# Optimization experiments

Hardware: AMD Instinct MI355X
Metric: run time of the kernel (lower is better)

Reference implementation:

```python
import jax, jax.numpy as jnp
import numpy as np

B, C, H, W = 8, 64, 48, 48
W_SCALE = 0.05  # ~1/sqrt(fan_in=128)


def conv1x1(x, w, b):
    # x: [B, Cin, H, W], w: [Cout, Cin], b: [Cout]
    return jnp.einsum('oc,bchw->bohw', w, x) + b[None, :, None, None]


def setup_inputs() -> dict:
    key = jax.random.key(0)
    ks = jax.random.split(key, 12)
    n = lambda k, s, sc=1.0: jax.random.normal(k, s, dtype=jnp.float32) * sc
    return {
        'xlh': n(ks[0], (B, C, H, W)),
        'xll': n(ks[1], (B, C, H, W)),
        'xrh': n(ks[2], (B, C, H, W)),
        'xrl': n(ks[3], (B, C, H, W)),
        'concaL_w': n(ks[4], (C, 2 * C), W_SCALE), 'concaL_b': jnp.zeros((C,), jnp.float32),
        'concaR_w': n(ks[5], (C, 2 * C), W_SCALE), 'concaR_b': jnp.zeros((C,), jnp.float32),
        'gateL_w': n(ks[6], (1, C), W_SCALE), 'gateL_b': jnp.zeros((1,), jnp.float32),
        'gateR_w': n(ks[7], (1, C), W_SCALE), 'gateR_b': jnp.zeros((1,), jnp.float32),
        'concaLo_w': n(ks[8], (C, 2 * C), W_SCALE), 'concaLo_b': jnp.zeros((C,), jnp.float32),
        'concaRo_w': n(ks[9], (C, 2 * C), W_SCALE), 'concaRo_b': jnp.zeros((C,), jnp.float32),
    }


def reference(xlh, xll, xrh, xrl,
              concaL_w, concaL_b, concaR_w, concaR_b,
              gateL_w, gateL_b, gateR_w, gateR_b,
              concaLo_w, concaLo_b, concaRo_w, concaRo_b):
    xL = conv1x1(jnp.concatenate([xlh, xll], axis=1), concaL_w, concaL_b)  # [B,C,H,W]
    xR = conv1x1(jnp.concatenate([xrh, xrl], axis=1), concaR_w, concaR_b)
    bs, ch, hei, wei = xL.shape
    hw = hei * wei
    xLr = xL.reshape(bs, ch, hw)  # [B,C,HW]
    xRr = xR.reshape(bs, ch, hw)
    # Affinity = xL^T xR : [B, HW_L, HW_R]
    aff = jnp.einsum('bcn,bcm->bnm', xLr, xRr)
    a1 = jax.nn.softmax(aff, axis=1)  # softmax over left positions
    a2 = jax.nn.softmax(aff, axis=2)  # softmax over right positions
    # Branch1: xL @ a1 -> [B,C,HW]
    b1 = jnp.einsum('bcn,bnm->bcm', xLr, a1).reshape(bs, ch, hei, wei)
    g1 = jax.nn.sigmoid(conv1x1(b1, gateL_w, gateL_b))  # [B,1,H,W]
    b1 = b1 * g1
    # Branch2: xR @ a2 -> [B,C,HW]
    b2 = jnp.einsum('bcn,bnm->bcm', xRr, a2).reshape(bs, ch, hei, wei)
    g2 = jax.nn.sigmoid(conv1x1(b2, gateR_w, gateR_b))
    b2 = b2 * g2
    out_L = conv1x1(jnp.concatenate([xL, b1], axis=1), concaLo_w, concaLo_b)
    out_R = conv1x1(jnp.concatenate([xR, b2], axis=1), concaRo_w, concaRo_b)
    return (out_L, out_R)
```

## Files before the change

### kernel.cpp

```cpp
#include <hip/hip_runtime.h>

typedef unsigned short u16;
typedef __bf16 bf16_t;
typedef bf16_t bf16x8 __attribute__((ext_vector_type(8)));
typedef float f32x4 __attribute__((ext_vector_type(4)));

#define B_   8
#define CH   64
#define HW   2304
#define L2E  1.4426950408889634f

#define OFF_XLC   0u
#define OFF_XRC   2359296u
#define OFF_XLT   4718592u
#define OFF_XRT   7077888u
#define OFF_B1    9437184u
#define OFF_B2    14155776u
#define OFF_RS2   18874368u

__device__ __forceinline__ float bf2f(u16 u){
  union { unsigned int i; float f; } v; v.i = ((unsigned int)u) << 16; return v.f;
}
__device__ __forceinline__ u16 f2bf(float f){
  union { float f; unsigned int i; } v; v.f = f;
  unsigned int r = v.i + 0x7FFFu + ((v.i >> 16) & 1u);
  return (u16)(r >> 16);
}
__device__ __forceinline__ void gload16(const void* g, void* l){
  __builtin_amdgcn_global_load_lds(
      (const __attribute__((address_space(1))) void*)g,
      (__attribute__((address_space(3))) void*)l, 16, 0, 0);
}

__global__ __launch_bounds__(256) void k_proj(
    const float* xlh, const float* xll, const float* xrh, const float* xrl,
    const float* wLl, const float* bLl, const float* wRr, const float* bRr,
    char* ws)
{
  int bid = blockIdx.x;
  int b   = bid & 7;
  int q   = bid >> 3;
  int o0  = (q & 3) * 16;
  int side= (q >> 2) & 1;
  int p   = (q >> 3) * 256 + threadIdx.x;
  const float* xh = (side ? xrh : xlh) + (size_t)b*CH*HW;
  const float* xl = (side ? xrl : xll) + (size_t)b*CH*HW;
  const float* w  = (side ? wRr : wLl);
  const float* bi = (side ? bRr : bLl);

  float acc[16];
  #pragma unroll
  for (int j=0;j<16;j++) acc[j] = bi[o0+j];
  for (int c=0;c<64;c++){
    float xv = xh[(size_t)c*HW + p];
    #pragma unroll
    for (int j=0;j<16;j++) acc[j] = fmaf(w[(size_t)(o0+j)*128 + c], xv, acc[j]);
  }
  for (int c=0;c<64;c++){
    float xv = xl[(size_t)c*HW + p];
    #pragma unroll
    for (int j=0;j<16;j++) acc[j] = fmaf(w[(size_t)(o0+j)*128 + 64 + c], xv, acc[j]);
  }
  u16* xc = (u16*)(ws + (side ? OFF_XRC : OFF_XLC)) + (size_t)b*CH*HW;
  u16* xt = (u16*)(ws + (side ? OFF_XRT : OFF_XLT)) + (size_t)b*HW*CH;
  unsigned int pk[8];
  #pragma unroll
  for (int j=0;j<8;j++){
    unsigned int lo16 = f2bf(acc[2*j]);
    unsigned int hi16 = f2bf(acc[2*j+1]);
    pk[j] = lo16 | (hi16 << 16);
    xc[(size_t)(o0+2*j  )*HW + p] = (u16)lo16;
    xc[(size_t)(o0+2*j+1)*HW + p] = (u16)hi16;
  }
  uint4* dst = (uint4*)&xt[(size_t)p*CH + o0];
  dst[0] = make_uint4(pk[0],pk[1],pk[2],pk[3]);
  dst[1] = make_uint4(pk[4],pk[5],pk[6],pk[7]);
}

__global__ __launch_bounds__(256, 4) void k_stats(char* ws)
{
  __shared__ alignas(16) char smraw[16384];
  __shared__ float part[4][4][4];
  int bid = blockIdx.x;
  int b   = bid & 7;
  int r0  = (bid >> 3) * 16;
  const char* Xb = ws + OFF_XLT + (size_t)b*HW*CH*2;
  const char* Yb = ws + OFF_XRT + (size_t)b*HW*CH*2;
  float* out = (float*)(ws + OFF_RS2) + b*HW;

  int lane = threadIdx.x & 63;
  int wv   = __builtin_amdgcn_readfirstlane(threadIdx.x >> 6);
  int lo = lane & 15, g = lane >> 4;
  int l = lane;

  const u16* Xu = (const u16*)Xb;
  bf16x8 a0 = *(const bf16x8*)&Xu[(size_t)(r0+lo)*CH + 8*g];
  bf16x8 a1 = *(const bf16x8*)&Xu[(size_t)(r0+lo)*CH + 32 + 8*g];

  int ySrc[2];
  #pragma unroll
  for (int j=0;j<2;j++){
    int r = j*8 + (l>>3);
    ySrc[j] = r*128 + (((l&7) ^ (r&7)))*16;
  }
  char* myY = smraw + wv*4096;
  int jbP = wv*576, jbQ = jbP + 288;

  int rdP0 = lo*128 + ((g      ^ (lo&7)))*16;
  int rdP1 = lo*128 + (((4|g)  ^ (lo&7)))*16;

  #define STAGE_S(i) do { \
    const char* gp = Yb + (size_t)(jbP + (i)*16)*128; \
    const char* gq = Yb + (size_t)(jbQ + (i)*16)*128; \
    gload16(gp + ySrc[0], myY + 0);    gload16(gp + ySrc[1], myY + 1024); \
    gload16(gq + ySrc[0], myY + 2048); gload16(gq + ySrc[1], myY + 3072); \
  } while(0)

  float sP[4] = {0.f,0.f,0.f,0.f};
  float sQ[4] = {0.f,0.f,0.f,0.f};

  STAGE_S(0);
  for (int i = 0; i < 18; ++i){
    asm volatile("s_waitcnt vmcnt(0)" ::: "memory");
    __builtin_amdgcn_sched_barrier(0);
    bf16x8 bP0 = *(const bf16x8*)(myY + rdP0);
    bf16x8 bP1 = *(const bf16x8*)(myY + rdP1);
    bf16x8 bQ0 = *(const bf16x8*)(myY + 2048 + rdP0);
    bf16x8 bQ1 = *(const bf16x8*)(myY + 2048 + rdP1);
    asm volatile("s_waitcnt lgkmcnt(0)" ::: "memory");
    __builtin_amdgcn_sched_barrier(0);
    int inext = (i+1 < 18) ? i+1 : 0;
    STAGE_S(inext);
    __builtin_amdgcn_sched_barrier(0);
    f32x4 z4 = {0.f,0.f,0.f,0.f};
    f32x4 dP = __builtin_amdgcn_mfma_f32_16x16x32_bf16(a0, bP0, z4, 0,0,0);
    dP = __builtin_amdgcn_mfma_f32_16x16x32_bf16(a1, bP1, dP, 0,0,0);
    f32x4 dQ = __builtin_amdgcn_mfma_f32_16x16x32_bf16(a0, bQ0, z4, 0,0,0);
    dQ = __builtin_amdgcn_mfma_f32_16x16x32_bf16(a1, bQ1, dQ, 0,0,0);
    #pragma unroll
    for (int r=0;r<4;r++){ sP[r] += exp2f(dP[r]*L2E); sQ[r] += exp2f(dQ[r]*L2E); }
  }
  #undef STAGE_S
  float s[4];
  #pragma unroll
  for (int r=0;r<4;r++) s[r] = sP[r] + sQ[r];
  #pragma unroll
  for (int mask = 1; mask < 16; mask <<= 1){
    #pragma unroll
    for (int r=0;r<4;r++) s[r] += __shfl_xor(s[r], mask, 64);
  }
  if (lo == 0){
    #pragma unroll
    for (int r=0;r<4;r++) part[wv][g][r] = s[r];
  }
  __syncthreads();
  if (threadIdx.x < 16){
    int t = threadIdx.x;
    float sum = part[0][t>>2][t&3] + part[1][t>>2][t&3]
              + part[2][t>>2][t&3] + part[3][t>>2][t&3];
    out[r0 + t] = 1.0f / sum;
  }
}

__global__ __launch_bounds__(256, 3) void k_attn(char* ws)
{
  __shared__ alignas(16) char smraw[49152];
  int bid  = blockIdx.x;
  int b    = bid & 7;
  int m0   = (bid >> 3) * 32;
  int lane = threadIdx.x & 63;
  int wv   = __builtin_amdgcn_readfirstlane(threadIdx.x >> 6);
  int lo = lane & 15, g = lane >> 4;
  int l = lane;

  const char* XLt = ws + OFF_XLT + (size_t)b*HW*CH*2;
  const char* XRt = ws + OFF_XRT + (size_t)b*HW*CH*2;
  const char* XLc = ws + OFF_XLC + (size_t)b*CH*HW*2;
  const char* XRc = ws + OFF_XRC + (size_t)b*CH*HW*2;
  const float* rs2 = (const float*)(ws + OFF_RS2) + b*HW;

  const u16* XRtu = (const u16*)XRt;
  bf16x8 fmA0 = *(const bf16x8*)&XRtu[(size_t)(m0+lo)*CH + 8*g];
  bf16x8 fmA1 = *(const bf16x8*)&XRtu[(size_t)(m0+lo)*CH + 32 + 8*g];
  bf16x8 fmB0 = *(const bf16x8*)&XRtu[(size_t)(m0+16+lo)*CH + 8*g];
  bf16x8 fmB1 = *(const bf16x8*)&XRtu[(size_t)(m0+16+lo)*CH + 32 + 8*g];

  int aSrc[4], bSrc[4];
  #pragma unroll
  for (int j=0;j<4;j++){
    int r  = j*8 + (l>>3);
    int sa = (r&3) | (((r>>3)&1)<<2);
    aSrc[j] = r*128 + (((l&7) ^ sa))*16;
    int c  = j*16 + (l>>2);
    int sb = (c>>1)&3;
    bSrc[j] = c*(HW*2) + (((l&3) ^ sb))*16;
  }
  char* myA  = smraw + wv*12288;
  char* myBL = myA + 4096;
  char* myBR = myA + 8192;

  int pr  = ((lo>>2)<<3) + (lo&3);
  int sAr = (lo&3) | (((lo>>2)&1)<<2);
  int rdA00 = pr*128     + ((g     ^ sAr))*16;
  int rdA01 = pr*128     + (((4|g) ^ sAr))*16;
  int rdA10 = (pr+4)*128 + ((g     ^ sAr))*16;
  int rdA11 = (pr+4)*128 + (((4|g) ^ sAr))*16;
  int sBr = (lo>>1)&3;
  int rdB0 = (     lo)*64 + ((g ^ sBr))*16;
  int rdB1 = (16 + lo)*64 + ((g ^ sBr))*16;
  int rdB2 = (32 + lo)*64 + ((g ^ sBr))*16;
  int rdB3 = (48 + lo)*64 + ((g ^ sBr))*16;

  #define STAGE_A(n0v) do { \
    const char* gA = XLt + (size_t)(n0v)*128; \
    const char* gL = XLc + (size_t)(n0v)*2; \
    const char* gR = XRc + (size_t)(n0v)*2; \
    gload16(gA + aSrc[0], myA  + 0);    gload16(gA + aSrc[1], myA  + 1024); \
    gload16(gA + aSrc[2], myA  + 2048); gload16(gA + aSrc[3], myA  + 3072); \
    gload16(gL + bSrc[0], myBL + 0);    gload16(gL + bSrc[1], myBL + 1024); \
    gload16(gL + bSrc[2], myBL + 2048); gload16(gL + bSrc[3], myBL + 3072); \
    gload16(gR + bSrc[0], myBR + 0);    gload16(gR + bSrc[1], myBR + 1024); \
    gload16(gR + bSrc[2], myBR + 2048); gload16(gR + bSrc[3], myBR + 3072); \
  } while(0)

  f32x4 acc1A[4], acc2A[4], acc1B[4], acc2B[4];
  #pragma unroll
  for (int ct=0;ct<4;ct++){
    f32x4 z4 = {0.f,0.f,0.f,0.f};
    acc1A[ct]=z4; acc2A[ct]=z4; acc1B[ct]=z4; acc2B[ct]=z4;
  }
  float s1A = 0.f, s1B = 0.f;

  int nbeg = wv * 576;
  STAGE_A(nbeg);
  for (int s = 0; s < 18; ++s){
    int n0 = nbeg + s*32;
    asm volatile("s_waitcnt vmcnt(0)" ::: "memory");
    __builtin_amdgcn_sched_barrier(0);
    bf16x8 fa00 = *(const bf16x8*)(myA + rdA00);
    bf16x8 fa01 = *(const bf16x8*)(myA + rdA01);
    bf16x8 fa10 = *(const bf16x8*)(myA + rdA10);
    bf16x8 fa11 = *(const bf16x8*)(myA + rdA11);
    bf16x8 bL0 = *(const bf16x8*)(myBL + rdB0);
    bf16x8 bL1 = *(const bf16x8*)(myBL + rdB1);
    bf16x8 bL2 = *(const bf16x8*)(myBL + rdB2);
    bf16x8 bL3 = *(const bf16x8*)(myBL + rdB3);
    bf16x8 bR0 = *(const bf16x8*)(myBR + rdB0);
    bf16x8 bR1 = *(const bf16x8*)(myBR + rdB1);
    bf16x8 bR2 = *(const bf16x8*)(myBR + rdB2);
    bf16x8 bR3 = *(const bf16x8*)(myBR + rdB3);
    f32x4 r20 = *(const f32x4*)&rs2[n0 + 8*g];
    f32x4 r21 = *(const f32x4*)&rs2[n0 + 8*g + 4];
    asm volatile("s_waitcnt lgkmcnt(0)" ::: "memory");
    __builtin_amdgcn_sched_barrier(0);
    int n1 = (s+1 < 18) ? n0 + 32 : nbeg;
    STAGE_A(n1);
    __builtin_amdgcn_sched_barrier(0);

    f32x4 z4 = {0.f,0.f,0.f,0.f};
    f32x4 d0A = __builtin_amdgcn_mfma_f32_16x16x32_bf16(fa00, fmA0, z4, 0,0,0);
    d0A = __builtin_amdgcn_mfma_f32_16x16x32_bf16(fa01, fmA1, d0A, 0,0,0);
    f32x4 d1A = __builtin_amdgcn_mfma_f32_16x16x32_bf16(fa10, fmA0, z4, 0,0,0);
    d1A = __builtin_amdgcn_mfma_f32_16x16x32_bf16(fa11, fmA1, d1A, 0,0,0);
    f32x4 d0B = __builtin_amdgcn_mfma_f32_16x16x32_bf16(fa00, fmB0, z4, 0,0,0);
    d0B = __builtin_amdgcn_mfma_f32_16x16x32_bf16(fa01, fmB1, d0B, 0,0,0);
    f32x4 d1B = __builtin_amdgcn_mfma_f32_16x16x32_bf16(fa10, fmB0, z4, 0,0,0);
    d1B = __builtin_amdgcn_mfma_f32_16x16x32_bf16(fa11, fmB1, d1B, 0,0,0);

    bf16x8 pa1A, pa2A, pa1B, pa2B;
    #pragma unroll
    for (int r=0;r<4;r++){
      float e0 = exp2f(d0A[r]*L2E);
      float e1 = exp2f(d1A[r]*L2E);
      s1A += e0 + e1;
      pa1A[r]   = (bf16_t)e0;
      pa1A[r+4] = (bf16_t)e1;
      pa2A[r]   = (bf16_t)(e0 * r20[r]);
      pa2A[r+4] = (bf16_t)(e1 * r21[r]);
      float f0 = exp2f(d0B[r]*L2E);
      float f1 = exp2f(d1B[r]*L2E);
      s1B += f0 + f1;
      pa1B[r]   = (bf16_t)f0;
      pa1B[r+4] = (bf16_t)f1;
      pa2B[r]   = (bf16_t)(f0 * r20[r]);
      pa2B[r+4] = (bf16_t)(f1 * r21[r]);
    }
    acc1A[0] = __builtin_amdgcn_mfma_f32_16x16x32_bf16(pa1A, bL0, acc1A[0], 0,0,0);
    acc1A[1] = __builtin_amdgcn_mfma_f32_16x16x32_bf16(pa1A, bL1, acc1A[1], 0,0,0);
    acc1A[2] = __builtin_amdgcn_mfma_f32_16x16x32_bf16(pa1A, bL2, acc1A[2], 0,0,0);
    acc1A[3] = __builtin_amdgcn_mfma_f32_16x16x32_bf16(pa1A, bL3, acc1A[3], 0,0,0);
    acc2A[0] = __builtin_amdgcn_mfma_f32_16x16x32_bf16(pa2A, bR0, acc2A[0], 0,0,0);
    acc2A[1] = __builtin_amdgcn_mfma_f32_16x16x32_bf16(pa2A, bR1, acc2A[1], 0,0,0);
    acc2A[2] = __builtin_amdgcn_mfma_f32_16x16x32_bf16(pa2A, bR2, acc2A[2], 0,0,0);
    acc2A[3] = __builtin_amdgcn_mfma_f32_16x16x32_bf16(pa2A, bR3, acc2A[3], 0,0,0);
    acc1B[0] = __builtin_amdgcn_mfma_f32_16x16x32_bf16(pa1B, bL0, acc1B[0], 0,0,0);
    acc1B[1] = __builtin_amdgcn_mfma_f32_16x16x32_bf16(pa1B, bL1, acc1B[1], 0,0,0);
    acc1B[2] = __builtin_amdgcn_mfma_f32_16x16x32_bf16(pa1B, bL2, acc1B[2], 0,0,0);
    acc1B[3] = __builtin_amdgcn_mfma_f32_16x16x32_bf16(pa1B, bL3, acc1B[3], 0,0,0);
    acc2B[0] = __builtin_amdgcn_mfma_f32_16x16x32_bf16(pa2B, bR0, acc2B[0], 0,0,0);
    acc2B[1] = __builtin_amdgcn_mfma_f32_16x16x32_bf16(pa2B, bR1, acc2B[1], 0,0,0);
    acc2B[2] = __builtin_amdgcn_mfma_f32_16x16x32_bf16(pa2B, bR2, acc2B[2], 0,0,0);
    acc2B[3] = __builtin_amdgcn_mfma_f32_16x16x32_bf16(pa2B, bR3, acc2B[3], 0,0,0);
  }
  #undef STAGE_A

  asm volatile("s_waitcnt vmcnt(0)" ::: "memory");
  __syncthreads();

  float (*red)[64][17] = (float (*)[64][17])smraw;
  float (*s1part)[32]  = (float (*)[32])(smraw + 17408);
  float* rs1inv        = (float*)(smraw + 17920);

  float s1Ar = s1A + __shfl_xor(s1A, 16, 64);
  s1Ar += __shfl_xor(s1Ar, 32, 64);
  float s1Br = s1B + __shfl_xor(s1B, 16, 64);
  s1Br += __shfl_xor(s1Br, 32, 64);
  if (lane < 16){ s1part[wv][lane] = s1Ar; s1part[wv][16+lane] = s1Br; }
  __syncthreads();
  if (threadIdx.x < 32){
    int t = threadIdx.x;
    float s = s1part[0][t] + s1part[1][t] + s1part[2][t] + s1part[3][t];
    rs1inv[t] = 1.0f / s;
  }
  __syncthreads();

  float* B1 = (float*)(ws + OFF_B1) + (size_t)b*CH*HW;
  float* B2 = (float*)(ws + OFF_B2) + (size_t)b*CH*HW;
  int rl = threadIdx.x & 63;
  int rv = threadIdx.x >> 6;

  #pragma unroll
  for (int v=0; v<16; ++v) red[wv][lane][v] = acc1A[v>>2][v&3];
  __syncthreads();
  #pragma unroll
  for (int k=0;k<4;k++){
    int v = rv + 4*k;
    float s = red[0][rl][v] + red[1][rl][v] + red[2][rl][v] + red[3][rl][v];
    int midx = ((rl>>4)<<2) + (v&3);
    int c = ((v>>2)<<4) + (rl & 15);
    B1[(size_t)c*HW + m0 + midx] = s * rs1inv[midx];
  }
  __syncthreads();
  #pragma unroll
  for (int v=0; v<16; ++v) red[wv][lane][v] = acc2A[v>>2][v&3];
  __syncthreads();
  #pragma unroll
  for (int k=0;k<4;k++){
    int v = rv + 4*k;
    float s = red[0][rl][v] + red[1][rl][v] + red[2][rl][v] + red[3][rl][v];
    int midx = ((rl>>4)<<2) + (v&3);
    int c = ((v>>2)<<4) + (rl & 15);
    B2[(size_t)c*HW + m0 + midx] = s;
  }
  __syncthreads();
  #pragma unroll
  for (int v=0; v<16; ++v) red[wv][lane][v] = acc1B[v>>2][v&3];
  __syncthreads();
  #pragma unroll
  for (int k=0;k<4;k++){
    int v = rv + 4*k;
    float s = red[0][rl][v] + red[1][rl][v] + red[2][rl][v] + red[3][rl][v];
    int midx = ((rl>>4)<<2) + (v&3);
    int c = ((v>>2)<<4) + (rl & 15);
    B1[(size_t)c*HW + m0 + 16 + midx] = s * rs1inv[16 + midx];
  }
  __syncthreads();
  #pragma unroll
  for (int v=0; v<16; ++v) red[wv][lane][v] = acc2B[v>>2][v&3];
  __syncthreads();
  #pragma unroll
  for (int k=0;k<4;k++){
    int v = rv + 4*k;
    float s = red[0][rl][v] + red[1][rl][v] + red[2][rl][v] + red[3][rl][v];
    int midx = ((rl>>4)<<2) + (v&3);
    int c = ((v>>2)<<4) + (rl & 15);
    B2[(size_t)c*HW + m0 + 16 + midx] = s;
  }
}

__global__ __launch_bounds__(256) void k_out(
    char* ws,
    const float* gwL, const float* gbL, const float* gwR, const float* gbR,
    const float* wLo, const float* bLoi, const float* wRo, const float* bRoi,
    float* out)
{
  __shared__ float xT[64][64];
  __shared__ float bT[64][64];
  __shared__ float gpart[4][64];
  __shared__ float gLds[64];
  int bid = blockIdx.x;
  int b   = bid & 7;
  int q   = bid >> 3;
  int side= q & 1;
  int p0  = (q >> 1) * 64;
  int t = threadIdx.x;
  const float* braw = (const float*)(ws + (side ? OFF_B2 : OFF_B1)) + (size_t)b*CH*HW;
  const u16*   xc   = (const u16*)(ws + (side ? OFF_XRC : OFF_XLC)) + (size_t)b*CH*HW;
  const float* w    = side ? wRo : wLo;
  const float* gw   = side ? gwR : gwL;
  float        gb   = side ? gbR[0] : gbL[0];
  const float* bias = side ? bRoi : bLoi;

  #pragma unroll
  for (int i=0;i<16;i++){
    int flat = i*256 + t;
    int c = flat >> 6, pl = flat & 63;
    bT[c][pl] = braw[(size_t)c*HW + p0 + pl];
    xT[c][pl] = bf2f(xc[(size_t)c*HW + p0 + pl]);
  }
  __syncthreads();
  {
    int qq = t >> 6, pl = t & 63;
    float a = 0.f;
    #pragma unroll
    for (int c = 0; c < 16; c++) a = fmaf(gw[16*qq + c], bT[16*qq + c][pl], a);
    gpart[qq][pl] = a;
  }
  __syncthreads();
  if (t < 64){
    float x = gpart[0][t]+gpart[1][t]+gpart[2][t]+gpart[3][t] + gb;
    gLds[t] = 1.0f/(1.0f + exp2f(-x*L2E));
  }
  __syncthreads();
  #pragma unroll
  for (int i=0;i<16;i++){
    int flat = i*256 + t;
    int c = flat >> 6, pl = flat & 63;
    bT[c][pl] *= gLds[pl];
  }
  __syncthreads();
  int wv = t >> 6;
  int lane = t & 63;
  float* outp = out + ((size_t)side*B_ + b)*CH*HW;

  float acc[16];
  #pragma unroll
  for (int oi=0;oi<16;oi++) acc[oi] = bias[wv*16 + oi];
  for (int c=0;c<64;c++){
    float xv = xT[c][lane];
    float bv = bT[c][lane];
    #pragma unroll
    for (int oi=0;oi<16;oi++){
      int o = wv*16 + oi;
      acc[oi] = fmaf(w[(size_t)o*128 + c],      xv, acc[oi]);
      acc[oi] = fmaf(w[(size_t)o*128 + 64 + c], bv, acc[oi]);
    }
  }
  #pragma unroll
  for (int oi=0;oi<16;oi++){
    int o = wv*16 + oi;
    outp[(size_t)o*HW + p0 + lane] = acc[oi];
  }
}

extern "C" void kernel_launch(void* const* d_in, const int* in_sizes, int n_in,
                              void* d_out, int out_size, void* d_ws, size_t ws_size,
                              hipStream_t stream)
{
  char* ws = (char*)d_ws;
  k_proj <<<576, 256, 0, stream>>>(
      (const float*)d_in[0], (const float*)d_in[1],
      (const float*)d_in[2], (const float*)d_in[3],
      (const float*)d_in[4], (const float*)d_in[5],
      (const float*)d_in[6], (const float*)d_in[7], ws);
  k_stats<<<1152, 256, 0, stream>>>(ws);
  k_attn <<<576, 256, 0, stream>>>(ws);
  k_out  <<<576, 256, 0, stream>>>(
      ws,
      (const float*)d_in[8],  (const float*)d_in[9],
      (const float*)d_in[10], (const float*)d_in[11],
      (const float*)d_in[12], (const float*)d_in[13],
      (const float*)d_in[14], (const float*)d_in[15],
      (float*)d_out);
}
```

Measured before the change: 160.6 us.

## Stage projection inputs in LDS and double row tile per stats block

The projection kernel now loads a 128-channel by 64-pixel input tile into shared memory once per block. Each wave then computes 16 output channels from that tile, so the input is no longer re-read from global memory once per output group. The stats kernel now processes 32 left rows per block instead of 16, reusing each staged right tile for twice the MFMA and exp work and halving the grid to 576 blocks. The cost is more registers in k_stats and fewer blocks to spread across the GPU.

```diff
diff --git a/kernel.cpp b/kernel.cpp
--- a/kernel.cpp
+++ b/kernel.cpp
@@ -37,29 +37,38 @@
     const float* wLl, const float* bLl, const float* wRr, const float* bRr,
     char* ws)
 {
+  __shared__ float xs[128][64];
   int bid = blockIdx.x;
   int b   = bid & 7;
   int q   = bid >> 3;
-  int o0  = (q & 3) * 16;
-  int side= (q >> 2) & 1;
-  int p   = (q >> 3) * 256 + threadIdx.x;
+  int side= q & 1;
+  int p0  = (q >> 1) * 64;
+  int t   = threadIdx.x;
   const float* xh = (side ? xrh : xlh) + (size_t)b*CH*HW;
   const float* xl = (side ? xrl : xll) + (size_t)b*CH*HW;
   const float* w  = (side ? wRr : wLl);
   const float* bi = (side ? bRr : bLl);
 
+  #pragma unroll
+  for (int i=0;i<8;i++){
+    int flat = i*256 + t;
+    int row  = flat >> 4;
+    int c4   = flat & 15;
+    const float* src = (row < 64) ? &xh[(size_t)row*HW + p0 + c4*4]
+                                  : &xl[(size_t)(row-64)*HW + p0 + c4*4];
+    *(float4*)&xs[row][c4*4] = *(const float4*)src;
+  }
+  __syncthreads();
+
+  int wv = t >> 6, lane = t & 63;
+  int o0 = wv*16;
   float acc[16];
   #pragma unroll
   for (int j=0;j<16;j++) acc[j] = bi[o0+j];
-  for (int c=0;c<64;c++){
-    float xv = xh[(size_t)c*HW + p];
+  for (int c=0;c<128;c++){
+    float xv = xs[c][lane];
     #pragma unroll
     for (int j=0;j<16;j++) acc[j] = fmaf(w[(size_t)(o0+j)*128 + c], xv, acc[j]);
-  }
-  for (int c=0;c<64;c++){
-    float xv = xl[(size_t)c*HW + p];
-    #pragma unroll
-    for (int j=0;j<16;j++) acc[j] = fmaf(w[(size_t)(o0+j)*128 + 64 + c], xv, acc[j]);
   }
   u16* xc = (u16*)(ws + (side ? OFF_XRC : OFF_XLC)) + (size_t)b*CH*HW;
   u16* xt = (u16*)(ws + (side ? OFF_XRT : OFF_XLT)) + (size_t)b*HW*CH;
@@ -69,10 +78,10 @@
     unsigned int lo16 = f2bf(acc[2*j]);
     unsigned int hi16 = f2bf(acc[2*j+1]);
     pk[j] = lo16 | (hi16 << 16);
-    xc[(size_t)(o0+2*j  )*HW + p] = (u16)lo16;
-    xc[(size_t)(o0+2*j+1)*HW + p] = (u16)hi16;
-  }
-  uint4* dst = (uint4*)&xt[(size_t)p*CH + o0];
+    xc[(size_t)(o0+2*j  )*HW + p0 + lane] = (u16)lo16;
+    xc[(size_t)(o0+2*j+1)*HW + p0 + lane] = (u16)hi16;
+  }
+  uint4* dst = (uint4*)&xt[(size_t)(p0+lane)*CH + o0];
   dst[0] = make_uint4(pk[0],pk[1],pk[2],pk[3]);
   dst[1] = make_uint4(pk[4],pk[5],pk[6],pk[7]);
 }
@@ -80,10 +89,10 @@
 __global__ __launch_bounds__(256, 4) void k_stats(char* ws)
 {
   __shared__ alignas(16) char smraw[16384];
-  __shared__ float part[4][4][4];
+  __shared__ float part[4][2][4][4];
   int bid = blockIdx.x;
   int b   = bid & 7;
-  int r0  = (bid >> 3) * 16;
+  int r0  = (bid >> 3) * 32;
   const char* Xb = ws + OFF_XLT + (size_t)b*HW*CH*2;
   const char* Yb = ws + OFF_XRT + (size_t)b*HW*CH*2;
   float* out = (float*)(ws + OFF_RS2) + b*HW;
@@ -94,8 +103,10 @@
   int l = lane;
 
   const u16* Xu = (const u16*)Xb;
-  bf16x8 a0 = *(const bf16x8*)&Xu[(size_t)(r0+lo)*CH + 8*g];
-  bf16x8 a1 = *(const bf16x8*)&Xu[(size_t)(r0+lo)*CH + 32 + 8*g];
+  bf16x8 aA0 = *(const bf16x8*)&Xu[(size_t)(r0+lo)*CH + 8*g];
+  bf16x8 aA1 = *(const bf16x8*)&Xu[(size_t)(r0+lo)*CH + 32 + 8*g];
+  bf16x8 aB0 = *(const bf16x8*)&Xu[(size_t)(r0+16+lo)*CH + 8*g];
+  bf16x8 aB1 = *(const bf16x8*)&Xu[(size_t)(r0+16+lo)*CH + 32 + 8*g];
 
   int ySrc[2];
   #pragma unroll
@@ -116,8 +127,10 @@
     gload16(gq + ySrc[0], myY + 2048); gload16(gq + ySrc[1], myY + 3072); \
   } while(0)
 
-  float sP[4] = {0.f,0.f,0.f,0.f};
-  float sQ[4] = {0.f,0.f,0.f,0.f};
+  float sPA[4] = {0.f,0.f,0.f,0.f};
+  float sQA[4] = {0.f,0.f,0.f,0.f};
+  float sPB[4] = {0.f,0.f,0.f,0.f};
+  float sQB[4] = {0.f,0.f,0.f,0.f};
 
   STAGE_S(0);
   for (int i = 0; i < 18; ++i){
@@ -133,32 +146,43 @@
     STAGE_S(inext);
     __builtin_amdgcn_sched_barrier(0);
     f32x4 z4 = {0.f,0.f,0.f,0.f};
-    f32x4 dP = __builtin_amdgcn_mfma_f32_16x16x32_bf16(a0, bP0, z4, 0,0,0);
-    dP = __builtin_amdgcn_mfma_f32_16x16x32_bf16(a1, bP1, dP, 0,0,0);
-    f32x4 dQ = __builtin_amdgcn_mfma_f32_16x16x32_bf16(a0, bQ0, z4, 0,0,0);
-    dQ = __builtin_amdgcn_mfma_f32_16x16x32_bf16(a1, bQ1, dQ, 0,0,0);
-    #pragma unroll
-    for (int r=0;r<4;r++){ sP[r] += exp2f(dP[r]*L2E); sQ[r] += exp2f(dQ[r]*L2E); }
+    f32x4 dPA = __builtin_amdgcn_mfma_f32_16x16x32_bf16(aA0, bP0, z4, 0,0,0);
+    dPA = __builtin_amdgcn_mfma_f32_16x16x32_bf16(aA1, bP1, dPA, 0,0,0);
+    f32x4 dQA = __builtin_amdgcn_mfma_f32_16x16x32_bf16(aA0, bQ0, z4, 0,0,0);
+    dQA = __builtin_amdgcn_mfma_f32_16x16x32_bf16(aA1, bQ1, dQA, 0,0,0);
+    f32x4 dPB = __builtin_amdgcn_mfma_f32_16x16x32_bf16(aB0, bP0, z4, 0,0,0);
+    dPB = __builtin_amdgcn_mfma_f32_16x16x32_bf16(aB1, bP1, dPB, 0,0,0);
+    f32x4 dQB = __builtin_amdgcn_mfma_f32_16x16x32_bf16(aB0, bQ0, z4, 0,0,0);
+    dQB = __builtin_amdgcn_mfma_f32_16x16x32_bf16(aB1, bQ1, dQB, 0,0,0);
+    #pragma unroll
+    for (int r=0;r<4;r++){
+      sPA[r] += exp2f(dPA[r]*L2E); sQA[r] += exp2f(dQA[r]*L2E);
+      sPB[r] += exp2f(dPB[r]*L2E); sQB[r] += exp2f(dQB[r]*L2E);
+    }
   }
   #undef STAGE_S
-  float s[4];
-  #pragma unroll
-  for (int r=0;r<4;r++) s[r] = sP[r] + sQ[r];
+  float sA[4], sB[4];
+  #pragma unroll
+  for (int r=0;r<4;r++){ sA[r] = sPA[r] + sQA[r]; sB[r] = sPB[r] + sQB[r]; }
   #pragma unroll
   for (int mask = 1; mask < 16; mask <<= 1){
     #pragma unroll
-    for (int r=0;r<4;r++) s[r] += __shfl_xor(s[r], mask, 64);
+    for (int r=0;r<4;r++){
+      sA[r] += __shfl_xor(sA[r], mask, 64);
+      sB[r] += __shfl_xor(sB[r], mask, 64);
+    }
   }
   if (lo == 0){
     #pragma unroll
-    for (int r=0;r<4;r++) part[wv][g][r] = s[r];
-  }
-  __syncthreads();
-  if (threadIdx.x < 16){
+    for (int r=0;r<4;r++){ part[wv][0][g][r] = sA[r]; part[wv][1][g][r] = sB[r]; }
+  }
+  __syncthreads();
+  if (threadIdx.x < 32){
     int t = threadIdx.x;
-    float sum = part[0][t>>2][t&3] + part[1][t>>2][t&3]
-              + part[2][t>>2][t&3] + part[3][t>>2][t&3];
-    out[r0 + t] = 1.0f / sum;
+    int half = t >> 4, gg = (t & 15) >> 2, rr = t & 3;
+    float sum = part[0][half][gg][rr] + part[1][half][gg][rr]
+              + part[2][half][gg][rr] + part[3][half][gg][rr];
+    out[r0 + 16*half + 4*gg + rr] = 1.0f / sum;
   }
 }
 
@@ -463,7 +487,7 @@
       (const float*)d_in[2], (const float*)d_in[3],
       (const float*)d_in[4], (const float*)d_in[5],
       (const float*)d_in[6], (const float*)d_in[7], ws);
-  k_stats<<<1152, 256, 0, stream>>>(ws);
+  k_stats<<<576, 256, 0, stream>>>(ws);
   k_attn <<<576, 256, 0, stream>>>(ws);
   k_out  <<<576, 256, 0, stream>>>(
       ws,
```

Measured after the change: 218.8 us. +36.2%, slower.
